# Optimization experiments

Measured on AMD Instinct MI355X. Metric: run time of the kernel, lower is better.

The kernel has to match this reference:

```python
import jax, jax.numpy as jnp
import numpy as np

HID = 2048
HEAD = 64
NH = HID // HEAD  # 32 heads
B, T = 4, 2048


def setup_inputs() -> dict:
    key = jax.random.key(0)
    ks = jax.random.split(key, 32)
    def n(i, shape, sc):
        return (jax.random.normal(ks[i], shape, jnp.float32) * sc).astype(jnp.float32)
    return {
        "hidden": n(0, (B, T, HID), 1.0),
        "attn_x": n(1, (B, HID), 1.0),
        "attn_kv": n(2, (B, NH, HEAD, HEAD), 0.1),
        "ffn_x": n(3, (B, HID), 1.0),
        "time_maa_x": n(4, (1, 1, HID), 0.5),
        "time_maa_w": n(5, (1, 1, HID), 0.5),
        "time_maa_k": n(6, (1, 1, HID), 0.5),
        "time_maa_v": n(7, (1, 1, HID), 0.5),
        "time_maa_r": n(8, (1, 1, HID), 0.5),
        "time_maa_g": n(9, (1, 1, HID), 0.5),
        "time_maa_w1": n(10, (HID, 160), 0.02),
        "time_maa_w2": n(11, (5, 32, HID), 0.02),
        "time_decay": n(12, (1, 1, HID), 0.5),
        "time_decay_w1": n(13, (HID, 64), 0.02),
        "time_decay_w2": n(14, (64, HID), 0.02),
        "time_faaaa": n(15, (NH, HEAD), 0.5),
        "receptance_w": n(16, (HID, HID), 0.02),
        "key_w": n(17, (HID, HID), 0.02),
        "value_w": n(18, (HID, HID), 0.02),
        "gate_w": n(19, (HID, HID), 0.02),
        "output_w": n(20, (HID, HID), 0.02),
        "gn_gamma": 1.0 + n(21, (HID,), 0.1),
        "gn_beta": n(22, (HID,), 0.1),
    }


def reference(hidden, attn_x, attn_kv, ffn_x,
              time_maa_x, time_maa_w, time_maa_k, time_maa_v, time_maa_r, time_maa_g,
              time_maa_w1, time_maa_w2, time_decay, time_decay_w1, time_decay_w2,
              time_faaaa, receptance_w, key_w, value_w, gate_w, output_w,
              gn_gamma, gn_beta):
    Bb, Tt, C = hidden.shape
    x = hidden
    shifted = jnp.concatenate([attn_x[:, None, :], x[:, :-1, :]], axis=1)
    dx = shifted - x
    time_mix = x + dx * time_maa_x
    # token-shift LoRA: (B,T,C)@(C,160) -> (5,B*T,32)@(5,32,C) -> five mixes
    xxx = jnp.tanh(time_mix @ time_maa_w1).reshape(Bb * Tt, 5, 32).transpose(1, 0, 2)
    xxx = jnp.einsum('nbk,nkc->nbc', xxx, time_maa_w2)
    mw, mk, mv, mr, mg = xxx.reshape(5, Bb, Tt, C)
    xw = x + dx * (time_maa_w + mw)
    xk = x + dx * (time_maa_k + mk)
    xv = x + dx * (time_maa_v + mv)
    xr = x + dx * (time_maa_r + mr)
    xg = x + dx * (time_maa_g + mg)
    r = (xr @ receptance_w).reshape(Bb, Tt, NH, HEAD).transpose(0, 2, 1, 3)  # (B,H,T,hs)
    k = (xk @ key_w).reshape(Bb, Tt, NH, HEAD).transpose(0, 2, 1, 3)
    v = (xv @ value_w).reshape(Bb, Tt, NH, HEAD).transpose(0, 2, 1, 3)
    g = jax.nn.silu(xg @ gate_w)
    td = time_decay + jnp.tanh(xw @ time_decay_w1) @ time_decay_w2  # (B,T,C)
    w = jnp.exp(-jnp.exp(td)).reshape(Bb, Tt, NH, HEAD).transpose(0, 2, 1, 3)
    # Source updates layer_state only AFTER the time loop, so inside the loop the
    # state is the constant attn_kv:  out_t = r_t @ (u * (k_t v_t^T) + S0).
    rk = jnp.einsum('bhtd,hd,bhtd->bht', r, time_faaaa, k)
    out = rk[..., None] * v + jnp.einsum('bhtd,bhde->bhte', r, attn_kv)  # (B,H,T,hs)
    new_attn_kv = k[:, :, -1, :, None] * v[:, :, -1, None, :] + w[:, :, -1, :, None] * attn_kv
    new_attn_x = hidden[:, -1]
    out = out.transpose(0, 2, 1, 3).reshape(Bb, Tt, C)
    # keras GroupNormalization(groups=NH) on (B,T,C): stats over (T, within-group channels)
    go = out.reshape(Bb, Tt, NH, HEAD)
    mean = go.mean(axis=(1, 3), keepdims=True)
    var = go.var(axis=(1, 3), keepdims=True)
    eps = 1e-5 * HEAD ** 2
    out = ((go - mean) * jax.lax.rsqrt(var + eps)).reshape(Bb, Tt, C) * gn_gamma + gn_beta
    out = (out * g) @ output_w
    return out, new_attn_x, new_attn_kv, ffn_x
```

## Files before the change

### kernel.cpp

```cpp
#include <hip/hip_runtime.h>

#define HID 2048
#define TSEQ 2048
#define BBATCH 4
#define MROWS 8192
#define NHEADS 32

typedef float fvec4 __attribute__((ext_vector_type(4)));
typedef unsigned short usvec4 __attribute__((ext_vector_type(4)));
typedef unsigned short usvec8 __attribute__((ext_vector_type(8)));
typedef __bf16 bh8 __attribute__((ext_vector_type(8)));
typedef float f32x4 __attribute__((ext_vector_type(4)));

__device__ __forceinline__ float bf2f(unsigned short u){
  return __uint_as_float(((unsigned int)u) << 16);
}
__device__ __forceinline__ unsigned short f2bf(float f){
  unsigned int u = __float_as_uint(f);
  return (unsigned short)((u + 0x7fffu + ((u >> 16) & 1u)) >> 16);
}
__device__ __forceinline__ void gll16(const void* g, void* lds){
  __builtin_amdgcn_global_load_lds(
      (const __attribute__((address_space(1))) unsigned int*)g,
      (__attribute__((address_space(3))) unsigned int*)lds, 16, 0, 0);
}

#define PIPE_SYNC(NSTR)                                              \
  asm volatile("s_waitcnt vmcnt(" NSTR ")\n\ts_barrier" ::: "memory"); \
  __builtin_amdgcn_sched_barrier(0);

__global__ void tcast6_kernel(const float* __restrict__ i0, const float* __restrict__ i1,
                              const float* __restrict__ i2, const float* __restrict__ i3,
                              const float* __restrict__ i4, const float* __restrict__ i5,
                              unsigned short* __restrict__ o0, unsigned short* __restrict__ o1,
                              unsigned short* __restrict__ o2, unsigned short* __restrict__ o3,
                              unsigned short* __restrict__ o4, unsigned short* __restrict__ o5){
  const float* in; unsigned short* out; int C = 2048;
  switch (blockIdx.z){
    case 0:  in = i0; out = o0; break;
    case 1:  in = i1; out = o1; break;
    case 2:  in = i2; out = o2; break;
    case 3:  in = i3; out = o3; break;
    case 4:  in = i4; out = o4; break;
    default: in = i5; out = o5; C = 160; break;
  }
  int c0 = blockIdx.x * 32, r0 = blockIdx.y * 32;
  if (c0 >= C) return;
  __shared__ float tile[32][33];
  int tx = threadIdx.x, ty = threadIdx.y;
  for (int i = ty; i < 32; i += 8){
    int c = c0 + tx;
    tile[i][tx] = (c < C) ? in[(size_t)(r0 + i) * C + c] : 0.f;
  }
  __syncthreads();
  for (int i = ty; i < 32; i += 8){
    int c = c0 + i;
    if (c < C) out[(size_t)c * 2048 + r0 + tx] = f2bf(tile[tx][i]);
  }
}

__global__ void tmix_kernel(const float* __restrict__ hidden, const float* __restrict__ attn_x,
                            const float* __restrict__ tmx, unsigned short* __restrict__ tm,
                            float* __restrict__ gsum, float* __restrict__ gsqs){
  if (blockIdx.x == 0 && threadIdx.x < 128){
    gsum[threadIdx.x] = 0.f;
    gsqs[threadIdx.x] = 0.f;
  }
  int i4 = blockIdx.x * 256 + threadIdx.x;
  int row = i4 >> 9;
  int c4 = i4 & 511;
  fvec4 x = *(const fvec4*)&hidden[(size_t)i4 * 4];
  fvec4 p;
  if ((row & (TSEQ - 1)) == 0){
    int b = row >> 11;
    p = *(const fvec4*)&attn_x[b * HID + c4 * 4];
  } else {
    p = *(const fvec4*)&hidden[(size_t)(i4 - 512) * 4];
  }
  fvec4 tx = *(const fvec4*)&tmx[c4 * 4];
  fvec4 t = x + (p - x) * tx;
  usvec4 o;
  o[0]=f2bf(t[0]); o[1]=f2bf(t[1]); o[2]=f2bf(t[2]); o[3]=f2bf(t[3]);
  *(usvec4*)&tm[(size_t)i4 * 4] = o;
}

template<int ACT, int OUTBF16>
__global__ __launch_bounds__(256, 2) void gemm_kernel(
    const unsigned short* __restrict__ A, const unsigned short* __restrict__ Bt,
    void* __restrict__ Cptr, int M, int N, int K, int ldc)
{
  __shared__ unsigned short As[128 * 32];
  __shared__ unsigned short Bs[128 * 32];
  const int tid = threadIdx.x;
  const int lane = tid & 63;
  const int w = tid >> 6;
  const int wr = w >> 1, wc = w & 1;
  const int lr = lane & 15, lq = lane >> 4;
  const int rowBase = blockIdx.y * 128;
  const int colBase = blockIdx.x * 128;

  const int arow = tid >> 2;
  const int ach = tid & 3;
  const unsigned short* aptr0 = A + (size_t)(rowBase + arow) * K + ach * 8;
  const unsigned short* aptr1 = aptr0 + (size_t)64 * K;
  int br0 = colBase + arow;      if (br0 > N - 1) br0 = N - 1;
  int br1 = colBase + arow + 64; if (br1 > N - 1) br1 = N - 1;
  const unsigned short* bptr0 = Bt + (size_t)br0 * K + ach * 8;
  const unsigned short* bptr1 = Bt + (size_t)br1 * K + ach * 8;

  f32x4 acc[4][4] = {};

  const int nk = K >> 5;
  for (int kk = 0; kk < nk; ++kk){
    gll16(aptr0, &As[tid * 8]);
    gll16(aptr1, &As[(tid + 256) * 8]);
    gll16(bptr0, &Bs[tid * 8]);
    gll16(bptr1, &Bs[(tid + 256) * 8]);
    aptr0 += 32; aptr1 += 32; bptr0 += 32; bptr1 += 32;
    __syncthreads();
    bh8 af[4], bfv[4];
    #pragma unroll
    for (int m = 0; m < 4; ++m)
      af[m] = *reinterpret_cast<const bh8*>(&As[(wr * 64 + m * 16 + lr) * 32 + lq * 8]);
    #pragma unroll
    for (int n = 0; n < 4; ++n)
      bfv[n] = *reinterpret_cast<const bh8*>(&Bs[(wc * 64 + n * 16 + lr) * 32 + lq * 8]);
    #pragma unroll
    for (int m = 0; m < 4; ++m)
      #pragma unroll
      for (int n = 0; n < 4; ++n)
        acc[m][n] = __builtin_amdgcn_mfma_f32_16x16x32_bf16(af[m], bfv[n], acc[m][n], 0, 0, 0);
    __syncthreads();
  }

  #pragma unroll
  for (int m = 0; m < 4; ++m){
    int gr0 = rowBase + wr * 64 + m * 16 + lq * 4;
    #pragma unroll
    for (int n = 0; n < 4; ++n){
      int gc = colBase + wc * 64 + n * 16 + lr;
      if (gc < N){
        #pragma unroll
        for (int q = 0; q < 4; ++q){
          float v = acc[m][n][q];
          if constexpr (ACT == 1) v = tanhf(v);
          else if constexpr (ACT == 2) v = v / (1.0f + __expf(-v));
          size_t off = (size_t)(gr0 + q) * ldc + gc;
          if constexpr (OUTBF16) ((unsigned short*)Cptr)[off] = f2bf(v);
          else                   ((float*)Cptr)[off] = v;
        }
      }
    }
  }
}

template<int OUTBF16>
__device__ __forceinline__ void gemm256_body(
    const unsigned short* __restrict__ A, const unsigned short* __restrict__ Bt,
    void* __restrict__ Cptr, int K, int act)
{
  __shared__ unsigned short smem[65536];
  const int tid = threadIdx.x;
  const int lane = tid & 63, w = tid >> 6;
  const int wr = w >> 2, wc = w & 3;
  const int lr = lane & 15, lq = lane >> 4;

  const int bid = blockIdx.y * gridDim.x + blockIdx.x;
  const int xcd = bid & 7, qq = bid >> 3;
  const int by = xcd * 4 + (qq >> 3);
  const int bx = qq & 7;
  const int rowBase = by * 256;
  const int colBase = bx * 256;
  const int N = gridDim.x * 256;

  const unsigned short* srcA[2]; const unsigned short* srcB[2];
  int dstA[2], dstB[2];
  #pragma unroll
  for (int l = 0; l < 2; ++l){
    int ci = l * 512 + tid;
    int r = ci >> 2, c = ci & 3;
    int g = c ^ ((r >> 1) & 3);
    srcA[l] = A  + (size_t)(rowBase + r) * K + g * 8;
    srcB[l] = Bt + (size_t)(colBase + r) * K + g * 8;
    dstA[l] = ci * 8;
    dstB[l] = 8192 + ci * 8;
  }

  f32x4 acc[8][4] = {};
  const int ksel = (lq ^ ((lr >> 1) & 3)) * 8;

  auto STAGE = [&](int t, int bi){
    unsigned short* buf = smem + bi * 16384;
    #pragma unroll
    for (int l = 0; l < 2; ++l){
      gll16(srcA[l] + (size_t)t * 32, buf + dstA[l]);
      gll16(srcB[l] + (size_t)t * 32, buf + dstB[l]);
    }
  };

  auto COMPUTE = [&](int bi){
    const unsigned short* aB = smem + bi * 16384;
    const unsigned short* bB = aB + 8192;
    bh8 af[8], bf[4];
    #pragma unroll
    for (int m = 0; m < 8; ++m)
      af[m] = *reinterpret_cast<const bh8*>(&aB[(wr * 128 + m * 16 + lr) * 32 + ksel]);
    #pragma unroll
    for (int n = 0; n < 4; ++n)
      bf[n] = *reinterpret_cast<const bh8*>(&bB[(wc * 64 + n * 16 + lr) * 32 + ksel]);
    __builtin_amdgcn_s_setprio(1);
    #pragma unroll
    for (int m = 0; m < 8; ++m)
      #pragma unroll
      for (int n = 0; n < 4; ++n)
        acc[m][n] = __builtin_amdgcn_mfma_f32_16x16x32_bf16(af[m], bf[n], acc[m][n], 0, 0, 0);
    __builtin_amdgcn_s_setprio(0);
  };

  const int nt = K >> 5;
  STAGE(0, 0); STAGE(1, 1); STAGE(2, 2);
  PIPE_SYNC("8");
  for (int t = 0; t < nt - 3; ++t){
    STAGE(t + 3, (t + 3) & 3);
    COMPUTE(t & 3);
    PIPE_SYNC("8");
  }
  COMPUTE((nt - 3) & 3);
  PIPE_SYNC("4");
  COMPUTE((nt - 2) & 3);
  PIPE_SYNC("0");
  COMPUTE((nt - 1) & 3);

  #pragma unroll
  for (int m = 0; m < 8; ++m){
    int gr0 = rowBase + wr * 128 + m * 16 + lq * 4;
    #pragma unroll
    for (int n = 0; n < 4; ++n){
      int gc = colBase + wc * 64 + n * 16 + lr;
      #pragma unroll
      for (int q = 0; q < 4; ++q){
        float v = acc[m][n][q];
        if (act == 2) v = v / (1.0f + __expf(-v));
        size_t off = (size_t)(gr0 + q) * N + gc;
        if constexpr (OUTBF16) ((unsigned short*)Cptr)[off] = f2bf(v);
        else                   ((float*)Cptr)[off] = v;
      }
    }
  }
}

__global__ __launch_bounds__(512, 2) void gemm256x4_kernel(
    const unsigned short* __restrict__ A0, const unsigned short* __restrict__ A1,
    const unsigned short* __restrict__ A2, const unsigned short* __restrict__ A3,
    const unsigned short* __restrict__ B0, const unsigned short* __restrict__ B1,
    const unsigned short* __restrict__ B2, const unsigned short* __restrict__ B3,
    unsigned short* __restrict__ C0, unsigned short* __restrict__ C1,
    unsigned short* __restrict__ C2, unsigned short* __restrict__ C3, int K)
{
  const unsigned short* A; const unsigned short* Bt; unsigned short* C; int act = 0;
  switch (blockIdx.z){
    case 0:  A = A0; Bt = B0; C = C0; break;
    case 1:  A = A1; Bt = B1; C = C1; break;
    case 2:  A = A2; Bt = B2; C = C2; break;
    default: A = A3; Bt = B3; C = C3; act = 2; break;
  }
  gemm256_body<1>(A, Bt, C, K, act);
}

__global__ __launch_bounds__(512, 2) void gemm256f_kernel(
    const unsigned short* __restrict__ A, const unsigned short* __restrict__ Bt,
    float* __restrict__ C, int K)
{
  gemm256_body<0>(A, Bt, C, K, 0);
}

__global__ __launch_bounds__(256) void mix_kernel(
    const float* __restrict__ xxx, const float* __restrict__ hidden,
    const float* __restrict__ attn_x, const float* __restrict__ w2,
    const float* __restrict__ tmk, const float* __restrict__ tmv,
    const float* __restrict__ tmr, const float* __restrict__ tmg,
    unsigned short* __restrict__ xk, unsigned short* __restrict__ xv,
    unsigned short* __restrict__ xr, unsigned short* __restrict__ xg)
{
  __shared__ __attribute__((aligned(16))) unsigned short smem[20992];
  unsigned short* xs   = smem;
  unsigned short* w2t  = smem + 10752;
  unsigned short* out4 = smem;

  const int tid = threadIdx.x;
  const int r0 = blockIdx.y * 64, c0 = blockIdx.x * 64;
  const int w = tid >> 6, lane = tid & 63, lr = lane & 15, lq = lane >> 4;

  for (int idx = tid; idx < 64 * 40; idx += 256){
    int r = idx / 40, cq = idx - r * 40;
    fvec4 v = *(const fvec4*)&xxx[(size_t)(r0 + r) * 160 + cq * 4];
    usvec4 o;
    o[0]=f2bf(v[0]); o[1]=f2bf(v[1]); o[2]=f2bf(v[2]); o[3]=f2bf(v[3]);
    *(usvec4*)&xs[r * 168 + cq * 4] = o;
  }
  for (int idx = tid; idx < 4 * 32 * 16; idx += 256){
    int n = idx >> 9;
    int rem = idx & 511;
    int j = rem >> 4, cq = rem & 15;
    fvec4 v = *(const fvec4*)&w2[(size_t)((n + 1) * 32 + j) * HID + c0 + cq * 4];
    #pragma unroll
    for (int cc = 0; cc < 4; ++cc)
      w2t[(n * 64 + cq * 4 + cc) * 40 + j] = f2bf(v[cc]);
  }
  __syncthreads();

  f32x4 acc[4][4] = {};
  #pragma unroll
  for (int n = 0; n < 4; ++n){
    bh8 afr = *reinterpret_cast<const bh8*>(&xs[(w * 16 + lr) * 168 + (n + 1) * 32 + lq * 8]);
    #pragma unroll
    for (int ct = 0; ct < 4; ++ct){
      bh8 bfr = *reinterpret_cast<const bh8*>(&w2t[(n * 64 + ct * 16 + lr) * 40 + lq * 8]);
      acc[ct][n] = __builtin_amdgcn_mfma_f32_16x16x32_bf16(afr, bfr, acc[ct][n], 0, 0, 0);
    }
  }
  __syncthreads();

  #pragma unroll
  for (int ct = 0; ct < 4; ++ct){
    int gc = c0 + ct * 16 + lr;
    float tk_ = tmk[gc], tv_ = tmv[gc], tr_ = tmr[gc], tg_ = tmg[gc];
    #pragma unroll
    for (int q = 0; q < 4; ++q){
      int row64 = w * 16 + lq * 4 + q;
      int gr = r0 + row64;
      size_t rowoff = (size_t)gr * HID + gc;
      float xx = hidden[rowoff];
      float pp = ((gr & (TSEQ - 1)) == 0) ? attn_x[(gr >> 11) * HID + gc]
                                          : hidden[rowoff - HID];
      float dxv = pp - xx;
      int lo = row64 * 72 + ct * 16 + lr;
      out4[(0 * 64 * 72) + lo] = f2bf(xx + dxv * (tk_ + acc[ct][0][q]));
      out4[(1 * 64 * 72) + lo] = f2bf(xx + dxv * (tv_ + acc[ct][1][q]));
      out4[(2 * 64 * 72) + lo] = f2bf(xx + dxv * (tr_ + acc[ct][2][q]));
      out4[(3 * 64 * 72) + lo] = f2bf(xx + dxv * (tg_ + acc[ct][3][q]));
    }
  }
  __syncthreads();

  #pragma unroll
  for (int a = 0; a < 4; ++a){
    unsigned short* dst = (a == 0) ? xk : (a == 1) ? xv : (a == 2) ? xr : xg;
    #pragma unroll
    for (int pass = 0; pass < 2; ++pass){
      int row64 = pass * 32 + (tid >> 3);
      int c8 = (tid & 7) * 8;
      usvec8 v8 = *(const usvec8*)&out4[(a * 64 + row64) * 72 + c8];
      *(usvec8*)&dst[(size_t)(r0 + row64) * HID + c0 + c8] = v8;
    }
  }
}

__global__ __launch_bounds__(256) void attn_kernel(
    const unsigned short* __restrict__ rb, const unsigned short* __restrict__ kb,
    const unsigned short* __restrict__ vb, const float* __restrict__ attn_kv,
    const float* __restrict__ faaaa, unsigned short* __restrict__ out0b,
    float* __restrict__ gsum, float* __restrict__ gsqs)
{
  const int bh = blockIdx.y;
  const int b = bh >> 5, h = bh & 31;
  const int tid = threadIdx.x, lane = tid & 63, w = tid >> 6;
  const int lr = lane & 15, lq = lane >> 4;
  const int t0 = blockIdx.x * 256 + w * 64;
  const size_t rowbase = (size_t)(b * TSEQ + t0) * HID + h * 64;

  const float* akvp = attn_kv + (size_t)bh * 4096;
  bh8 bfr[2][4];
  #pragma unroll
  for (int kk = 0; kk < 2; ++kk)
    #pragma unroll
    for (int n = 0; n < 4; ++n)
      #pragma unroll
      for (int j = 0; j < 8; ++j)
        bfr[kk][n][j] = (__bf16)akvp[(kk * 32 + lq * 8 + j) * 64 + n * 16 + lr];

  float fa0[8], fa1[8];
  #pragma unroll
  for (int j = 0; j < 8; ++j){
    fa0[j] = faaaa[h * 64 + lq * 8 + j];
    fa1[j] = faaaa[h * 64 + 32 + lq * 8 + j];
  }

  __shared__ __attribute__((aligned(16))) float rk_s[4][64];
  __shared__ __attribute__((aligned(16))) unsigned short outb[4][64][72];

  f32x4 acc[4][4] = {};
  #pragma unroll
  for (int m = 0; m < 4; ++m){
    size_t ra = rowbase + (size_t)(m * 16 + lr) * HID;
    bh8 a0 = *reinterpret_cast<const bh8*>(&rb[ra + lq * 8]);
    bh8 a1 = *reinterpret_cast<const bh8*>(&rb[ra + 32 + lq * 8]);
    usvec8 k0 = *reinterpret_cast<const usvec8*>(&kb[ra + lq * 8]);
    usvec8 k1 = *reinterpret_cast<const usvec8*>(&kb[ra + 32 + lq * 8]);
    float p = 0.f;
    #pragma unroll
    for (int j = 0; j < 8; ++j){
      p += (float)a0[j] * fa0[j] * bf2f(k0[j]);
      p += (float)a1[j] * fa1[j] * bf2f(k1[j]);
    }
    p += __shfl_xor(p, 16, 64);
    p += __shfl_xor(p, 32, 64);
    if (lq == 0) rk_s[w][m * 16 + lr] = p;
    #pragma unroll
    for (int n = 0; n < 4; ++n){
      acc[m][n] = __builtin_amdgcn_mfma_f32_16x16x32_bf16(a0, bfr[0][n], acc[m][n], 0, 0, 0);
      acc[m][n] = __builtin_amdgcn_mfma_f32_16x16x32_bf16(a1, bfr[1][n], acc[m][n], 0, 0, 0);
    }
  }
  __syncthreads();

  float ssum = 0.f, ssq = 0.f;
  #pragma unroll
  for (int m = 0; m < 4; ++m){
    fvec4 rk4 = *(const fvec4*)&rk_s[w][m * 16 + lq * 4];
    #pragma unroll
    for (int n = 0; n < 4; ++n){
      int col = n * 16 + lr;
      #pragma unroll
      for (int q = 0; q < 4; ++q){
        int row = m * 16 + lq * 4 + q;
        float vv = bf2f(vb[rowbase + (size_t)row * HID + col]);
        float o = acc[m][n][q] + rk4[q] * vv;
        ssum += o; ssq += o * o;
        outb[w][row][col] = f2bf(o);
      }
    }
  }
  __syncthreads();
  #pragma unroll
  for (int pass = 0; pass < 8; ++pass){
    int row = pass * 8 + (lane >> 3);
    int c8 = (lane & 7) * 8;
    usvec8 o8 = *(const usvec8*)&outb[w][row][c8];
    *(usvec8*)&out0b[rowbase + (size_t)row * HID + c8] = o8;
  }
  #pragma unroll
  for (int off2 = 32; off2 > 0; off2 >>= 1){
    ssum += __shfl_xor(ssum, off2, 64);
    ssq  += __shfl_xor(ssq,  off2, 64);
  }
  if (lane == 0){ atomicAdd(&gsum[bh], ssum); atomicAdd(&gsqs[bh], ssq); }
}

__global__ void ynorm_kernel(const unsigned short* __restrict__ out0b,
                             const unsigned short* __restrict__ gb,
                             const float* __restrict__ gsum, const float* __restrict__ gsqs,
                             const float* __restrict__ gamma,
                             const float* __restrict__ beta, unsigned short* __restrict__ yb){
  int i4 = blockIdx.x * 256 + threadIdx.x;
  int row = i4 >> 9, c4 = i4 & 511;
  int b = row >> 11;
  int c = c4 * 4;
  int g = b * 32 + (c >> 6);
  const float rn = 1.0f / (float)(TSEQ * 64);
  float mean = gsum[g] * rn;
  float var  = gsqs[g] * rn - mean * mean;
  float inv  = rsqrtf(var + 1e-5f * 64.0f * 64.0f);
  usvec4 o4 = *(const usvec4*)&out0b[(size_t)i4 * 4];
  usvec4 gv = *(const usvec4*)&gb[(size_t)i4 * 4];
  fvec4 ga = *(const fvec4*)&gamma[c];
  fvec4 be = *(const fvec4*)&beta[c];
  usvec4 y;
  #pragma unroll
  for (int cc = 0; cc < 4; ++cc){
    float val = ((bf2f(o4[cc]) - mean) * inv * ga[cc] + be[cc]) * bf2f(gv[cc]);
    y[cc] = f2bf(val);
  }
  *(usvec4*)&yb[(size_t)i4 * 4] = y;
}

__global__ void lastrow_mix_kernel(const float* __restrict__ xxx, const float* __restrict__ hidden,
    const float* __restrict__ w2, const float* __restrict__ tmw, const float* __restrict__ tmk,
    const float* __restrict__ tmv, float* __restrict__ xw_l, float* __restrict__ xk_l,
    float* __restrict__ xv_l){
  int b = blockIdx.y;
  int c = blockIdx.x * 256 + threadIdx.x;
  __shared__ float xsr[160];
  int i = b * TSEQ + (TSEQ - 1);
  if (threadIdx.x < 160) xsr[threadIdx.x] = xxx[(size_t)i * 160 + threadIdx.x];
  __syncthreads();
  float mw = 0.f, mk = 0.f, mv = 0.f;
  for (int j = 0; j < 32; ++j){
    mw += xsr[j]      * w2[(size_t)(j)      * HID + c];
    mk += xsr[32 + j] * w2[(size_t)(32 + j) * HID + c];
    mv += xsr[64 + j] * w2[(size_t)(64 + j) * HID + c];
  }
  float x = hidden[(size_t)i * HID + c];
  float prev = hidden[(size_t)(i - 1) * HID + c];
  float dx = prev - x;
  xw_l[b * HID + c] = x + dx * (tmw[c] + mw);
  xk_l[b * HID + c] = x + dx * (tmk[c] + mk);
  xv_l[b * HID + c] = x + dx * (tmv[c] + mv);
}

__global__ void decay1_part_kernel(const float* __restrict__ xw_l, const float* __restrict__ tdw1,
                                   float* __restrict__ dpart){
  int b = blockIdx.y;
  int chunk = blockIdx.x;
  int j = threadIdx.x & 63, sub = threadIdx.x >> 6;
  float s = 0.f;
  int cbase = chunk * 128 + sub * 32;
  for (int r = 0; r < 32; ++r){
    int c = cbase + r;
    s += xw_l[b * HID + c] * tdw1[(size_t)c * 64 + j];
  }
  __shared__ float red[4][64];
  red[sub][j] = s;
  __syncthreads();
  if (sub == 0)
    dpart[((size_t)b * 16 + chunk) * 64 + j] = red[0][j] + red[1][j] + red[2][j] + red[3][j];
}

__global__ __launch_bounds__(256) void lastrow_kv_part_kernel(
    const float* __restrict__ xk_l, const float* __restrict__ xv_l,
    const float* __restrict__ keyw, const float* __restrict__ valw,
    float* __restrict__ kpart, float* __restrict__ vpart){
  int c = blockIdx.x * 256 + threadIdx.x;
  int chunk = blockIdx.y;
  __shared__ float xs[2][4][128];
  for (int i = threadIdx.x; i < 512; i += 256){
    int b = i >> 7, r = i & 127;
    xs[0][b][r] = xk_l[b * HID + chunk * 128 + r];
    xs[1][b][r] = xv_l[b * HID + chunk * 128 + r];
  }
  __syncthreads();
  float ka[4] = {0,0,0,0}, va[4] = {0,0,0,0};
  for (int r = 0; r < 128; ++r){
    int c2 = chunk * 128 + r;
    float kw = keyw[(size_t)c2 * HID + c];
    float vw = valw[(size_t)c2 * HID + c];
    #pragma unroll
    for (int b = 0; b < 4; ++b){
      ka[b] += xs[0][b][r] * kw;
      va[b] += xs[1][b][r] * vw;
    }
  }
  #pragma unroll
  for (int b = 0; b < 4; ++b){
    kpart[((size_t)chunk * 4 + b) * HID + c] = ka[b];
    vpart[((size_t)chunk * 4 + b) * HID + c] = va[b];
  }
}

__global__ void lastrow_kv_reduce_kernel(
    const float* __restrict__ kpart, const float* __restrict__ vpart,
    const float* __restrict__ dpart, const float* __restrict__ tdw2,
    const float* __restrict__ tdecay, float* __restrict__ klast,
    float* __restrict__ vlast, float* __restrict__ wlast){
  __shared__ float hdec_s[256];
  {
    int t = threadIdx.x;
    int b = t >> 6, j = t & 63;
    float s = 0.f;
    #pragma unroll
    for (int chunk = 0; chunk < 16; ++chunk)
      s += dpart[((size_t)b * 16 + chunk) * 64 + j];
    hdec_s[t] = tanhf(s);
  }
  __syncthreads();
  int c = blockIdx.x * 256 + threadIdx.x;
  float ka[4] = {0,0,0,0}, va[4] = {0,0,0,0};
  for (int chunk = 0; chunk < 16; ++chunk){
    #pragma unroll
    for (int b = 0; b < 4; ++b){
      ka[b] += kpart[((size_t)chunk * 4 + b) * HID + c];
      va[b] += vpart[((size_t)chunk * 4 + b) * HID + c];
    }
  }
  float tdc = tdecay[c];
  float td[4] = {tdc, tdc, tdc, tdc};
  for (int j = 0; j < 64; ++j){
    float w2v = tdw2[(size_t)j * HID + c];
    #pragma unroll
    for (int b = 0; b < 4; ++b) td[b] += hdec_s[b * 64 + j] * w2v;
  }
  #pragma unroll
  for (int b = 0; b < 4; ++b){
    klast[b * HID + c] = ka[b];
    vlast[b * HID + c] = va[b];
    wlast[b * HID + c] = expf(-expf(td[b]));
  }
}

__global__ void newkv_copies_kernel(const float* __restrict__ klast,
    const float* __restrict__ vlast, const float* __restrict__ wlast,
    const float* __restrict__ attn_kv, const float* __restrict__ hidden,
    const float* __restrict__ ffnx, float* __restrict__ outkv,
    float* __restrict__ out_attnx, float* __restrict__ out_ffnx){
  if (blockIdx.x < 2048){
    int idx = blockIdx.x * 256 + threadIdx.x;
    int b = idx >> 17;
    int h = (idx >> 12) & 31;
    int d = (idx >> 6) & 63;
    int e = idx & 63;
    float kl = klast[b * HID + h * 64 + d];
    float vl = vlast[b * HID + h * 64 + e];
    float wl = wlast[b * HID + h * 64 + d];
    outkv[idx] = kl * vl + wl * attn_kv[idx];
  } else {
    int i = (blockIdx.x - 2048) * 256 + threadIdx.x;
    int b = i >> 11, c = i & 2047;
    out_attnx[i] = hidden[((size_t)(b * TSEQ + TSEQ - 1)) * HID + c];
    out_ffnx[i] = ffnx[i];
  }
}

extern "C" void kernel_launch(void* const* d_in, const int* in_sizes, int n_in,
                              void* d_out, int out_size, void* d_ws, size_t ws_size,
                              hipStream_t stream)
{
  (void)in_sizes; (void)n_in; (void)out_size;
  const float* hidden = (const float*)d_in[0];
  const float* attn_x = (const float*)d_in[1];
  const float* attn_kv = (const float*)d_in[2];
  const float* ffn_x = (const float*)d_in[3];
  const float* tmaa_x = (const float*)d_in[4];
  const float* tmaa_w = (const float*)d_in[5];
  const float* tmaa_k = (const float*)d_in[6];
  const float* tmaa_v = (const float*)d_in[7];
  const float* tmaa_r = (const float*)d_in[8];
  const float* tmaa_g = (const float*)d_in[9];
  const float* w1 = (const float*)d_in[10];
  const float* w2 = (const float*)d_in[11];
  const float* tdecay = (const float*)d_in[12];
  const float* tdw1 = (const float*)d_in[13];
  const float* tdw2 = (const float*)d_in[14];
  const float* faaaa = (const float*)d_in[15];
  const float* recw = (const float*)d_in[16];
  const float* keyw = (const float*)d_in[17];
  const float* valw = (const float*)d_in[18];
  const float* gatew = (const float*)d_in[19];
  const float* outw = (const float*)d_in[20];
  const float* gamma = (const float*)d_in[21];
  const float* beta = (const float*)d_in[22];

  float* out_main  = (float*)d_out;
  float* out_attnx = out_main + (size_t)16777216;
  float* out_kv    = out_attnx + 8192;
  float* out_ffn   = out_kv + 524288;

  unsigned short* wr_t = (unsigned short*)d_out;
  unsigned short* wk_t = wr_t + (size_t)4194304;
  unsigned short* wv_t = wk_t + (size_t)4194304;
  unsigned short* wg_t = wv_t + (size_t)4194304;
  unsigned short* out0b = (unsigned short*)d_out;

  char* ws = (char*)d_ws;
  size_t off = 0;
  auto alloc = [&](size_t bytes) -> void* {
    void* p = ws + off; off += (bytes + 255) & ~(size_t)255; return p;
  };
  unsigned short* wo_t = (unsigned short*)alloc(2048ull * 2048 * 2);
  unsigned short* w1_t = (unsigned short*)alloc(160ull * 2048 * 2);
  float* xxx           = (float*)alloc((size_t)MROWS * 160 * 4);
  unsigned short* bufA = (unsigned short*)alloc((size_t)MROWS * HID * 2);
  unsigned short* bufB = (unsigned short*)alloc((size_t)MROWS * HID * 2);
  unsigned short* bufC = (unsigned short*)alloc((size_t)MROWS * HID * 2);
  unsigned short* bufD = (unsigned short*)alloc((size_t)MROWS * HID * 2);
  unsigned short* bufE = (unsigned short*)alloc((size_t)MROWS * HID * 2);
  float* gsum    = (float*)alloc(128 * 4);
  float* gsqs    = (float*)alloc(128 * 4);
  float* xw_l  = (float*)alloc(BBATCH * HID * 4);
  float* xk_l  = (float*)alloc(BBATCH * HID * 4);
  float* xv_l  = (float*)alloc(BBATCH * HID * 4);
  float* klast = (float*)alloc(BBATCH * HID * 4);
  float* vlast = (float*)alloc(BBATCH * HID * 4);
  float* wlast = (float*)alloc(BBATCH * HID * 4);
  float* kpart = (float*)alloc(16ull * BBATCH * HID * 4);
  float* vpart = (float*)alloc(16ull * BBATCH * HID * 4);
  float* dpart = (float*)alloc((size_t)BBATCH * 16 * 64 * 4);

  if (off > ws_size) return;

  unsigned short* tm = bufA;
  unsigned short* xg = bufA;
  unsigned short* xr = bufB;
  unsigned short* kb = bufB;
  unsigned short* yb = bufB;
  unsigned short* xk = bufC;
  unsigned short* vb = bufC;
  unsigned short* xv = bufD;
  unsigned short* gb = bufD;
  unsigned short* rb = bufE;

  dim3 tb(32, 8);
  tcast6_kernel<<<dim3(64, 64, 6), tb, 0, stream>>>(
      recw, keyw, valw, gatew, outw, w1,
      wr_t, wk_t, wv_t, wg_t, wo_t, w1_t);

  tmix_kernel<<<16384, 256, 0, stream>>>(hidden, attn_x, tmaa_x, tm, gsum, gsqs);

  gemm_kernel<1, 0><<<dim3(2, 64), 256, 0, stream>>>(tm, w1_t, xxx, MROWS, 160, HID, 160);

  mix_kernel<<<dim3(32, 128), 256, 0, stream>>>(xxx, hidden, attn_x, w2,
      tmaa_k, tmaa_v, tmaa_r, tmaa_g, xk, xv, xr, xg);

  gemm256x4_kernel<<<dim3(8, 32, 4), 512, 0, stream>>>(
      xr, xk, xv, xg, wr_t, wk_t, wv_t, wg_t, rb, kb, vb, gb, HID);

  attn_kernel<<<dim3(8, 128), 256, 0, stream>>>(rb, kb, vb, attn_kv, faaaa,
                                                out0b, gsum, gsqs);
  ynorm_kernel<<<16384, 256, 0, stream>>>(out0b, gb, gsum, gsqs, gamma, beta, yb);

  gemm256f_kernel<<<dim3(8, 32), 512, 0, stream>>>(yb, wo_t, out_main, HID);

  lastrow_mix_kernel<<<dim3(8, 4), 256, 0, stream>>>(xxx, hidden, w2, tmaa_w, tmaa_k, tmaa_v,
                                                     xw_l, xk_l, xv_l);
  decay1_part_kernel<<<dim3(16, 4), 256, 0, stream>>>(xw_l, tdw1, dpart);
  lastrow_kv_part_kernel<<<dim3(8, 16), 256, 0, stream>>>(xk_l, xv_l, keyw, valw, kpart, vpart);
  lastrow_kv_reduce_kernel<<<8, 256, 0, stream>>>(kpart, vpart, dpart, tdw2, tdecay,
                                                  klast, vlast, wlast);
  newkv_copies_kernel<<<2080, 256, 0, stream>>>(klast, vlast, wlast, attn_kv,
                                                hidden, ffn_x, out_kv,
                                                out_attnx, out_ffn);
}
```

Before: 643.5 us.

## Fold last-row state kernels into existing launches as extra blocks

Removes the five separate kernels that compute the final-token state (last-row mix, decay LoRA, k/v projections, reduction, new kv and copies). Their work is added as extra grid blocks that branch off at the start of the mix, batched GEMM, attention and norm kernels. This cuts launch count and the serialized tail of small kernels, letting that work overlap with the large kernels. In exchange, the GEMM and attention kernels carry extra shared memory and branch logic, which could affect occupancy or register allocation.

```diff
diff --git a/kernel.cpp b/kernel.cpp
--- a/kernel.cpp
+++ b/kernel.cpp
@@ -249,14 +249,80 @@
   }
 }
 
+__device__ void proj_tail(
+    const float* __restrict__ xw_l, const float* __restrict__ xk_l,
+    const float* __restrict__ xv_l, const float* __restrict__ tdw1,
+    const float* __restrict__ keyw, const float* __restrict__ valw,
+    float* __restrict__ dpart, float* __restrict__ kpart,
+    float* __restrict__ vpart)
+{
+  __shared__ float red[8][64];
+  __shared__ float xs[2][4][128];
+  const int bid = blockIdx.y * gridDim.x + blockIdx.x;
+  const int tid = threadIdx.x;
+  if (bid < 64){
+    int b = bid >> 4, chunk = bid & 15;
+    int j = tid & 63, sub = tid >> 6;
+    float s = 0.f;
+    int cbase = chunk * 128 + sub * 16;
+    for (int r = 0; r < 16; ++r){
+      int c = cbase + r;
+      s += xw_l[b * HID + c] * tdw1[(size_t)c * 64 + j];
+    }
+    red[sub][j] = s;
+    __syncthreads();
+    if (sub == 0){
+      float t = 0.f;
+      #pragma unroll
+      for (int k2 = 0; k2 < 8; ++k2) t += red[k2][j];
+      dpart[((size_t)b * 16 + chunk) * 64 + j] = t;
+    }
+  } else if (bid < 128){
+    int cb = bid - 64;
+    int chunk = cb >> 2, c4 = cb & 3;
+    int c = c4 * 512 + tid;
+    for (int i = tid; i < 1024; i += 512){
+      int a = i >> 9, rem = i & 511;
+      int b = rem >> 7, r = rem & 127;
+      xs[a][b][r] = (a == 0 ? xk_l : xv_l)[b * HID + chunk * 128 + r];
+    }
+    __syncthreads();
+    float ka[4] = {0,0,0,0}, va[4] = {0,0,0,0};
+    for (int r = 0; r < 128; ++r){
+      int c2 = chunk * 128 + r;
+      float kw = keyw[(size_t)c2 * HID + c];
+      float vw = valw[(size_t)c2 * HID + c];
+      #pragma unroll
+      for (int b = 0; b < 4; ++b){
+        ka[b] += xs[0][b][r] * kw;
+        va[b] += xs[1][b][r] * vw;
+      }
+    }
+    #pragma unroll
+    for (int b = 0; b < 4; ++b){
+      kpart[((size_t)chunk * 4 + b) * HID + c] = ka[b];
+      vpart[((size_t)chunk * 4 + b) * HID + c] = va[b];
+    }
+  }
+}
+
 __global__ __launch_bounds__(512, 2) void gemm256x4_kernel(
     const unsigned short* __restrict__ A0, const unsigned short* __restrict__ A1,
     const unsigned short* __restrict__ A2, const unsigned short* __restrict__ A3,
     const unsigned short* __restrict__ B0, const unsigned short* __restrict__ B1,
     const unsigned short* __restrict__ B2, const unsigned short* __restrict__ B3,
     unsigned short* __restrict__ C0, unsigned short* __restrict__ C1,
-    unsigned short* __restrict__ C2, unsigned short* __restrict__ C3, int K)
+    unsigned short* __restrict__ C2, unsigned short* __restrict__ C3, int K,
+    const float* __restrict__ xw_l, const float* __restrict__ xk_l,
+    const float* __restrict__ xv_l, const float* __restrict__ tdw1,
+    const float* __restrict__ keyw, const float* __restrict__ valw,
+    float* __restrict__ dpart, float* __restrict__ kpart,
+    float* __restrict__ vpart)
 {
+  if (blockIdx.z == 4){
+    proj_tail(xw_l, xk_l, xv_l, tdw1, keyw, valw, dpart, kpart, vpart);
+    return;
+  }
   const unsigned short* A; const unsigned short* Bt; unsigned short* C; int act = 0;
   switch (blockIdx.z){
     case 0:  A = A0; Bt = B0; C = C0; break;
@@ -279,10 +345,35 @@
     const float* __restrict__ attn_x, const float* __restrict__ w2,
     const float* __restrict__ tmk, const float* __restrict__ tmv,
     const float* __restrict__ tmr, const float* __restrict__ tmg,
+    const float* __restrict__ tmw,
     unsigned short* __restrict__ xk, unsigned short* __restrict__ xv,
-    unsigned short* __restrict__ xr, unsigned short* __restrict__ xg)
+    unsigned short* __restrict__ xr, unsigned short* __restrict__ xg,
+    float* __restrict__ xw_l, float* __restrict__ xk_l, float* __restrict__ xv_l)
 {
   __shared__ __attribute__((aligned(16))) unsigned short smem[20992];
+  __shared__ float xsr[160];
+
+  if (blockIdx.y == 128){
+    int b = blockIdx.x >> 3, cblk = blockIdx.x & 7;
+    int c = cblk * 256 + threadIdx.x;
+    int i = b * TSEQ + (TSEQ - 1);
+    if (threadIdx.x < 160) xsr[threadIdx.x] = xxx[(size_t)i * 160 + threadIdx.x];
+    __syncthreads();
+    float mw = 0.f, mk = 0.f, mv = 0.f;
+    for (int j = 0; j < 32; ++j){
+      mw += xsr[j]      * w2[(size_t)(j)      * HID + c];
+      mk += xsr[32 + j] * w2[(size_t)(32 + j) * HID + c];
+      mv += xsr[64 + j] * w2[(size_t)(64 + j) * HID + c];
+    }
+    float x = hidden[(size_t)i * HID + c];
+    float prev = hidden[(size_t)(i - 1) * HID + c];
+    float dx = prev - x;
+    xw_l[b * HID + c] = x + dx * (tmw[c] + mw);
+    xk_l[b * HID + c] = x + dx * (tmk[c] + mk);
+    xv_l[b * HID + c] = x + dx * (tmv[c] + mv);
+    return;
+  }
+
   unsigned short* xs   = smem;
   unsigned short* w2t  = smem + 10752;
   unsigned short* out4 = smem;
@@ -360,8 +451,53 @@
     const unsigned short* __restrict__ rb, const unsigned short* __restrict__ kb,
     const unsigned short* __restrict__ vb, const float* __restrict__ attn_kv,
     const float* __restrict__ faaaa, unsigned short* __restrict__ out0b,
-    float* __restrict__ gsum, float* __restrict__ gsqs)
+    float* __restrict__ gsum, float* __restrict__ gsqs,
+    const float* __restrict__ kpart, const float* __restrict__ vpart,
+    const float* __restrict__ dpart, const float* __restrict__ tdw2,
+    const float* __restrict__ tdecay, float* __restrict__ klast,
+    float* __restrict__ vlast, float* __restrict__ wlast)
 {
+  __shared__ __attribute__((aligned(16))) float rk_s[4][64];
+  __shared__ __attribute__((aligned(16))) unsigned short outb[4][64][72];
+  __shared__ float hdec_s[256];
+
+  if (blockIdx.x == 8){
+    if (blockIdx.y >= 8) return;
+    {
+      int t = threadIdx.x;
+      int b = t >> 6, j = t & 63;
+      float s = 0.f;
+      #pragma unroll
+      for (int chunk = 0; chunk < 16; ++chunk)
+        s += dpart[((size_t)b * 16 + chunk) * 64 + j];
+      hdec_s[t] = tanhf(s);
+    }
+    __syncthreads();
+    int c = blockIdx.y * 256 + threadIdx.x;
+    float ka[4] = {0,0,0,0}, va[4] = {0,0,0,0};
+    for (int chunk = 0; chunk < 16; ++chunk){
+      #pragma unroll
+      for (int b = 0; b < 4; ++b){
+        ka[b] += kpart[((size_t)chunk * 4 + b) * HID + c];
+        va[b] += vpart[((size_t)chunk * 4 + b) * HID + c];
+      }
+    }
+    float tdc = tdecay[c];
+    float td[4] = {tdc, tdc, tdc, tdc};
+    for (int j = 0; j < 64; ++j){
+      float w2v = tdw2[(size_t)j * HID + c];
+      #pragma unroll
+      for (int b = 0; b < 4; ++b) td[b] += hdec_s[b * 64 + j] * w2v;
+    }
+    #pragma unroll
+    for (int b = 0; b < 4; ++b){
+      klast[b * HID + c] = ka[b];
+      vlast[b * HID + c] = va[b];
+      wlast[b * HID + c] = expf(-expf(td[b]));
+    }
+    return;
+  }
+
   const int bh = blockIdx.y;
   const int b = bh >> 5, h = bh & 31;
   const int tid = threadIdx.x, lane = tid & 63, w = tid >> 6;
@@ -385,9 +521,6 @@
     fa0[j] = faaaa[h * 64 + lq * 8 + j];
     fa1[j] = faaaa[h * 64 + 32 + lq * 8 + j];
   }
-
-  __shared__ __attribute__((aligned(16))) float rk_s[4][64];
-  __shared__ __attribute__((aligned(16))) unsigned short outb[4][64][72];
 
   f32x4 acc[4][4] = {};
   #pragma unroll
@@ -451,7 +584,32 @@
                              const unsigned short* __restrict__ gb,
                              const float* __restrict__ gsum, const float* __restrict__ gsqs,
                              const float* __restrict__ gamma,
-                             const float* __restrict__ beta, unsigned short* __restrict__ yb){
+                             const float* __restrict__ beta, unsigned short* __restrict__ yb,
+                             const float* __restrict__ klast, const float* __restrict__ vlast,
+                             const float* __restrict__ wlast, const float* __restrict__ attn_kv,
+                             const float* __restrict__ hidden, const float* __restrict__ ffnx,
+                             float* __restrict__ outkv, float* __restrict__ out_attnx,
+                             float* __restrict__ out_ffnx){
+  if (blockIdx.x >= 16384){
+    int bx2 = blockIdx.x - 16384;
+    if (bx2 < 2048){
+      int idx = bx2 * 256 + threadIdx.x;
+      int b = idx >> 17;
+      int h = (idx >> 12) & 31;
+      int d = (idx >> 6) & 63;
+      int e = idx & 63;
+      float kl = klast[b * HID + h * 64 + d];
+      float vl = vlast[b * HID + h * 64 + e];
+      float wl = wlast[b * HID + h * 64 + d];
+      outkv[idx] = kl * vl + wl * attn_kv[idx];
+    } else {
+      int i = (bx2 - 2048) * 256 + threadIdx.x;
+      int b = i >> 11, c = i & 2047;
+      out_attnx[i] = hidden[((size_t)(b * TSEQ + TSEQ - 1)) * HID + c];
+      out_ffnx[i] = ffnx[i];
+    }
+    return;
+  }
   int i4 = blockIdx.x * 256 + threadIdx.x;
   int row = i4 >> 9, c4 = i4 & 511;
   int b = row >> 11;
@@ -472,142 +630,6 @@
     y[cc] = f2bf(val);
   }
   *(usvec4*)&yb[(size_t)i4 * 4] = y;
-}
-
-__global__ void lastrow_mix_kernel(const float* __restrict__ xxx, const float* __restrict__ hidden,
-    const float* __restrict__ w2, const float* __restrict__ tmw, const float* __restrict__ tmk,
-    const float* __restrict__ tmv, float* __restrict__ xw_l, float* __restrict__ xk_l,
-    float* __restrict__ xv_l){
-  int b = blockIdx.y;
-  int c = blockIdx.x * 256 + threadIdx.x;
-  __shared__ float xsr[160];
-  int i = b * TSEQ + (TSEQ - 1);
-  if (threadIdx.x < 160) xsr[threadIdx.x] = xxx[(size_t)i * 160 + threadIdx.x];
-  __syncthreads();
-  float mw = 0.f, mk = 0.f, mv = 0.f;
-  for (int j = 0; j < 32; ++j){
-    mw += xsr[j]      * w2[(size_t)(j)      * HID + c];
-    mk += xsr[32 + j] * w2[(size_t)(32 + j) * HID + c];
-    mv += xsr[64 + j] * w2[(size_t)(64 + j) * HID + c];
-  }
-  float x = hidden[(size_t)i * HID + c];
-  float prev = hidden[(size_t)(i - 1) * HID + c];
-  float dx = prev - x;
-  xw_l[b * HID + c] = x + dx * (tmw[c] + mw);
-  xk_l[b * HID + c] = x + dx * (tmk[c] + mk);
-  xv_l[b * HID + c] = x + dx * (tmv[c] + mv);
-}
-
-__global__ void decay1_part_kernel(const float* __restrict__ xw_l, const float* __restrict__ tdw1,
-                                   float* __restrict__ dpart){
-  int b = blockIdx.y;
-  int chunk = blockIdx.x;
-  int j = threadIdx.x & 63, sub = threadIdx.x >> 6;
-  float s = 0.f;
-  int cbase = chunk * 128 + sub * 32;
-  for (int r = 0; r < 32; ++r){
-    int c = cbase + r;
-    s += xw_l[b * HID + c] * tdw1[(size_t)c * 64 + j];
-  }
-  __shared__ float red[4][64];
-  red[sub][j] = s;
-  __syncthreads();
-  if (sub == 0)
-    dpart[((size_t)b * 16 + chunk) * 64 + j] = red[0][j] + red[1][j] + red[2][j] + red[3][j];
-}
-
-__global__ __launch_bounds__(256) void lastrow_kv_part_kernel(
-    const float* __restrict__ xk_l, const float* __restrict__ xv_l,
-    const float* __restrict__ keyw, const float* __restrict__ valw,
-    float* __restrict__ kpart, float* __restrict__ vpart){
-  int c = blockIdx.x * 256 + threadIdx.x;
-  int chunk = blockIdx.y;
-  __shared__ float xs[2][4][128];
-  for (int i = threadIdx.x; i < 512; i += 256){
-    int b = i >> 7, r = i & 127;
-    xs[0][b][r] = xk_l[b * HID + chunk * 128 + r];
-    xs[1][b][r] = xv_l[b * HID + chunk * 128 + r];
-  }
-  __syncthreads();
-  float ka[4] = {0,0,0,0}, va[4] = {0,0,0,0};
-  for (int r = 0; r < 128; ++r){
-    int c2 = chunk * 128 + r;
-    float kw = keyw[(size_t)c2 * HID + c];
-    float vw = valw[(size_t)c2 * HID + c];
-    #pragma unroll
-    for (int b = 0; b < 4; ++b){
-      ka[b] += xs[0][b][r] * kw;
-      va[b] += xs[1][b][r] * vw;
-    }
-  }
-  #pragma unroll
-  for (int b = 0; b < 4; ++b){
-    kpart[((size_t)chunk * 4 + b) * HID + c] = ka[b];
-    vpart[((size_t)chunk * 4 + b) * HID + c] = va[b];
-  }
-}
-
-__global__ void lastrow_kv_reduce_kernel(
-    const float* __restrict__ kpart, const float* __restrict__ vpart,
-    const float* __restrict__ dpart, const float* __restrict__ tdw2,
-    const float* __restrict__ tdecay, float* __restrict__ klast,
-    float* __restrict__ vlast, float* __restrict__ wlast){
-  __shared__ float hdec_s[256];
-  {
-    int t = threadIdx.x;
-    int b = t >> 6, j = t & 63;
-    float s = 0.f;
-    #pragma unroll
-    for (int chunk = 0; chunk < 16; ++chunk)
-      s += dpart[((size_t)b * 16 + chunk) * 64 + j];
-    hdec_s[t] = tanhf(s);
-  }
-  __syncthreads();
-  int c = blockIdx.x * 256 + threadIdx.x;
-  float ka[4] = {0,0,0,0}, va[4] = {0,0,0,0};
-  for (int chunk = 0; chunk < 16; ++chunk){
-    #pragma unroll
-    for (int b = 0; b < 4; ++b){
-      ka[b] += kpart[((size_t)chunk * 4 + b) * HID + c];
-      va[b] += vpart[((size_t)chunk * 4 + b) * HID + c];
-    }
-  }
-  float tdc = tdecay[c];
-  float td[4] = {tdc, tdc, tdc, tdc};
-  for (int j = 0; j < 64; ++j){
-    float w2v = tdw2[(size_t)j * HID + c];
-    #pragma unroll
-    for (int b = 0; b < 4; ++b) td[b] += hdec_s[b * 64 + j] * w2v;
-  }
-  #pragma unroll
-  for (int b = 0; b < 4; ++b){
-    klast[b * HID + c] = ka[b];
-    vlast[b * HID + c] = va[b];
-    wlast[b * HID + c] = expf(-expf(td[b]));
-  }
-}
-
-__global__ void newkv_copies_kernel(const float* __restrict__ klast,
-    const float* __restrict__ vlast, const float* __restrict__ wlast,
-    const float* __restrict__ attn_kv, const float* __restrict__ hidden,
-    const float* __restrict__ ffnx, float* __restrict__ outkv,
-    float* __restrict__ out_attnx, float* __restrict__ out_ffnx){
-  if (blockIdx.x < 2048){
-    int idx = blockIdx.x * 256 + threadIdx.x;
-    int b = idx >> 17;
-    int h = (idx >> 12) & 31;
-    int d = (idx >> 6) & 63;
-    int e = idx & 63;
-    float kl = klast[b * HID + h * 64 + d];
-    float vl = vlast[b * HID + h * 64 + e];
-    float wl = wlast[b * HID + h * 64 + d];
-    outkv[idx] = kl * vl + wl * attn_kv[idx];
-  } else {
-    int i = (blockIdx.x - 2048) * 256 + threadIdx.x;
-    int b = i >> 11, c = i & 2047;
-    out_attnx[i] = hidden[((size_t)(b * TSEQ + TSEQ - 1)) * HID + c];
-    out_ffnx[i] = ffnx[i];
-  }
 }
 
 extern "C" void kernel_launch(void* const* d_in, const int* in_sizes, int n_in,
@@ -697,25 +719,21 @@
 
   gemm_kernel<1, 0><<<dim3(2, 64), 256, 0, stream>>>(tm, w1_t, xxx, MROWS, 160, HID, 160);
 
-  mix_kernel<<<dim3(32, 128), 256, 0, stream>>>(xxx, hidden, attn_x, w2,
-      tmaa_k, tmaa_v, tmaa_r, tmaa_g, xk, xv, xr, xg);
-
-  gemm256x4_kernel<<<dim3(8, 32, 4), 512, 0, stream>>>(
-      xr, xk, xv, xg, wr_t, wk_t, wv_t, wg_t, rb, kb, vb, gb, HID);
-
-  attn_kernel<<<dim3(8, 128), 256, 0, stream>>>(rb, kb, vb, attn_kv, faaaa,
-                                                out0b, gsum, gsqs);
-  ynorm_kernel<<<16384, 256, 0, stream>>>(out0b, gb, gsum, gsqs, gamma, beta, yb);
+  mix_kernel<<<dim3(32, 129), 256, 0, stream>>>(xxx, hidden, attn_x, w2,
+      tmaa_k, tmaa_v, tmaa_r, tmaa_g, tmaa_w, xk, xv, xr, xg, xw_l, xk_l, xv_l);
+
+  gemm256x4_kernel<<<dim3(8, 32, 5), 512, 0, stream>>>(
+      xr, xk, xv, xg, wr_t, wk_t, wv_t, wg_t, rb, kb, vb, gb, HID,
+      xw_l, xk_l, xv_l, tdw1, keyw, valw, dpart, kpart, vpart);
+
+  attn_kernel<<<dim3(9, 128), 256, 0, stream>>>(rb, kb, vb, attn_kv, faaaa,
+                                                out0b, gsum, gsqs,
+                                                kpart, vpart, dpart, tdw2, tdecay,
+                                                klast, vlast, wlast);
+
+  ynorm_kernel<<<18464, 256, 0, stream>>>(out0b, gb, gsum, gsqs, gamma, beta, yb,
+                                          klast, vlast, wlast, attn_kv,
+                                          hidden, ffn_x, out_kv, out_attnx, out_ffn);
 
   gemm256f_kernel<<<dim3(8, 32), 512, 0, stream>>>(yb, wo_t, out_main, HID);
-
-  lastrow_mix_kernel<<<dim3(8, 4), 256, 0, stream>>>(xxx, hidden, w2, tmaa_w, tmaa_k, tmaa_v,
-                                                     xw_l, xk_l, xv_l);
-  decay1_part_kernel<<<dim3(16, 4), 256, 0, stream>>>(xw_l, tdw1, dpart);
-  lastrow_kv_part_kernel<<<dim3(8, 16), 256, 0, stream>>>(xk_l, xv_l, keyw, valw, kpart, vpart);
-  lastrow_kv_reduce_kernel<<<8, 256, 0, stream>>>(kpart, vpart, dpart, tdw2, tdecay,
-                                                  klast, vlast, wlast);
-  newkv_copies_kernel<<<2080, 256, 0, stream>>>(klast, vlast, wlast, attn_kv,
-                                                hidden, ffn_x, out_kv,
-                                                out_attnx, out_ffn);
-}
+}
```

After: 673.7 us. 4.7% more time.
